# Kernel tuning notes

Hardware: AMD Instinct MI355X
Metric: run time of the kernel (lower is better)

## Reference

```python
import jax, jax.numpy as jnp
import numpy as np

B, T, D_IN, P, Q, D_OUT = 128, 1024, 64, 128, 2, 64


def _lstm_layer(x, w_ih, w_hh, b):
    """One LSTM layer, batch_first. x: [B,T,Din], w_ih: [4P,Din], w_hh: [4P,P], b: [4P].
    PyTorch gate order: i, f, g, o."""
    # Precompute input contribution for all timesteps (the big, parallel GEMM).
    gx = jnp.einsum('btd,gd->btg', x, w_ih) + b          # [B,T,4P]
    gx_t = jnp.swapaxes(gx, 0, 1)                        # [T,B,4P] for scan
    p = w_hh.shape[1]
    h0 = jnp.zeros((x.shape[0], p), dtype=x.dtype)
    c0 = jnp.zeros((x.shape[0], p), dtype=x.dtype)

    def step(carry, g_in):
        h, c = carry
        g = g_in + h @ w_hh.T                            # [B,4P]
        i, f, gg, o = jnp.split(g, 4, axis=-1)
        i = jax.nn.sigmoid(i)
        f = jax.nn.sigmoid(f)
        gg = jnp.tanh(gg)
        o = jax.nn.sigmoid(o)
        c = f * c + i * gg
        h = o * jnp.tanh(c)
        return (h, c), h

    _, hs = jax.lax.scan(step, (h0, c0), gx_t)           # hs: [T,B,P]
    return jnp.swapaxes(hs, 0, 1)                        # [B,T,P]


def setup_inputs() -> dict:
    key = jax.random.key(0)
    ks = jax.random.split(key, 8)
    x = jax.random.normal(ks[0], (B, T, D_IN), dtype=jnp.float32)
    # weight_ih: kaiming-normal-ish; weight_hh: orthogonal-ish (random normal is a fine stand-in
    # numerically; init distribution doesn't change the math being tested).
    w_ih0 = jax.random.normal(ks[1], (4 * P, D_IN), dtype=jnp.float32) * (1.0 / np.sqrt(D_IN))
    w_hh0 = jax.random.normal(ks[2], (4 * P, P), dtype=jnp.float32) * (1.0 / np.sqrt(P))
    w_ih1 = jax.random.normal(ks[3], (4 * P, P), dtype=jnp.float32) * (1.0 / np.sqrt(P))
    w_hh1 = jax.random.normal(ks[4], (4 * P, P), dtype=jnp.float32) * (1.0 / np.sqrt(P))
    # biases initialized to zero in the original (bias_ih + bias_hh folded into one per layer
    # would be equivalent math; keep both for faithfulness)
    b_ih = jnp.zeros((Q, 4 * P), dtype=jnp.float32)
    b_hh = jnp.zeros((Q, 4 * P), dtype=jnp.float32)
    fc_w = jax.random.normal(ks[5], (D_OUT, P), dtype=jnp.float32) * np.sqrt(2.0 / P)
    fc_b = jnp.zeros((D_OUT,), dtype=jnp.float32)
    return {"x": x, "w_ih0": w_ih0, "w_hh0": w_hh0, "w_ih1": w_ih1, "w_hh1": w_hh1,
            "b_ih": b_ih, "b_hh": b_hh, "fc_w": fc_w, "fc_b": fc_b}


def reference(x, w_ih0, w_hh0, w_ih1, w_hh1, b_ih, b_hh, fc_w, fc_b):
    h = _lstm_layer(x, w_ih0, w_hh0, b_ih[0] + b_hh[0])   # layer 0: [B,T,P]
    h = _lstm_layer(h, w_ih1, w_hh1, b_ih[1] + b_hh[1])   # layer 1: [B,T,P]
    return jnp.einsum('btp,op->bto', h, fc_w) + fc_b      # [B,T,D_OUT]
```

## Files before the change

### kernel.cpp

```cpp
#include <hip/hip_runtime.h>

#define NT 1024
#define RING 256
#define RMAR 24

typedef _Float16 half8 __attribute__((ext_vector_type(8)));
typedef _Float16 half4 __attribute__((ext_vector_type(4)));
typedef float f32x4 __attribute__((ext_vector_type(4)));

__device__ __forceinline__ f32x4 MFMA(half8 a, half8 b, f32x4 c) {
  return __builtin_amdgcn_mfma_f32_16x16x32_f16(a, b, c, 0, 0, 0);
}
__device__ __forceinline__ float sigf(float x) {
  return __builtin_amdgcn_rcpf(1.0f + __expf(-x));
}
__device__ __forceinline__ float tanhf2(float x) {
  float ax = fabsf(x);
  float e = __expf(-2.0f * ax);
  float t = (1.0f - e) * __builtin_amdgcn_rcpf(1.0f + e);
  return copysignf(t, x);
}
__device__ __forceinline__ half8 cvt8(float4 c0, float4 c1) {
  half8 hv;
  hv[0] = (_Float16)c0.x; hv[1] = (_Float16)c0.y;
  hv[2] = (_Float16)c0.z; hv[3] = (_Float16)c0.w;
  hv[4] = (_Float16)c1.x; hv[5] = (_Float16)c1.y;
  hv[6] = (_Float16)c1.z; hv[7] = (_Float16)c1.w;
  return hv;
}
struct U2 { unsigned long long a, b; };

__global__ __launch_bounds__(256) void prep_x(const float* __restrict__ x,
                                              _Float16* __restrict__ Xf) {
  int t0 = blockIdx.x * 256 + threadIdx.x;
  int l = t0 & 63;
  int fid = t0 >> 6;
  int kt = fid & 1;
  int t = (fid >> 1) & (NT - 1);
  int g = fid >> 11;
  int bt = g * 16 + (l & 15);
  int kb = kt * 32 + (l >> 4) * 4;
  const float* src = x + ((size_t)bt * NT + (size_t)t) * 64 + kb;
  float4 v0 = *(const float4*)src;
  float4 v1 = *(const float4*)(src + 16);
  *(half8*)(Xf + (size_t)fid * 512 + l * 8) = cvt8(v0, v1);
}

__global__ __launch_bounds__(512, 2) void lstm_main(
    const float* __restrict__ wih0, const float* __restrict__ whh0,
    const float* __restrict__ wih1, const float* __restrict__ whh1,
    const float* __restrict__ bih, const float* __restrict__ bhh,
    const float* __restrict__ fcw, const float* __restrict__ fcb,
    const _Float16* __restrict__ Xf, _Float16* __restrict__ ring,
    unsigned* __restrict__ prog, unsigned* __restrict__ consread,
    float* __restrict__ out) {
  const int tid = threadIdx.x;
  const int w = tid >> 6, l = tid & 63;
  const int n = l & 15, lg = l >> 4;
  const bool producer = blockIdx.x < 8;
  const int g = blockIdx.x & 7;

  __shared__ _Float16 hfrag[2][4][64][8];

  if (tid < 256) {
    half8 z = {0, 0, 0, 0, 0, 0, 0, 0};
    ((half8*)&hfrag[1][0][0][0])[tid] = z;
  }

  if (producer) {
    half8 A[4][6];
    f32x4 bias[4];
#pragma unroll
    for (int q = 0; q < 4; ++q) {
      int row = (w + 8 * q) * 16 + n;
#pragma unroll
      for (int kt = 0; kt < 6; ++kt) {
        int kb = kt * 32 + lg * 4;
        const float* wp = (kt < 2) ? (wih0 + (size_t)row * 64 + kb)
                                   : (whh0 + (size_t)row * 128 + (kb - 64));
        A[q][kt] = cvt8(*(const float4*)wp, *(const float4*)(wp + 16));
      }
      int rb = (w + 8 * q) * 16 + lg * 4;
      f32x4 bv;
#pragma unroll
      for (int r = 0; r < 4; ++r) bv[r] = bih[rb + r] + bhh[rb + r];
      bias[q] = bv;
    }
    const _Float16* XfG = Xf + (size_t)g * NT * 1024;
    _Float16* ringG = ring + (size_t)g * RING * 2048;
    half8 x0 = *(const half8*)(XfG + l * 8);
    half8 x1 = *(const half8*)(XfG + 512 + l * 8);
    f32x4 cst = {0.f, 0.f, 0.f, 0.f};
    unsigned Cc = 0;
    __syncthreads();
    for (int s = 0; s < NT; ++s) {
      half8 xn0, xn1;
      if (s + 1 < NT) {
        const _Float16* p = XfG + (size_t)(s + 1) * 1024 + l * 8;
        xn0 = *(const half8*)p;
        xn1 = *(const half8*)(p + 512);
      }
      if ((s & 7) == 0 && s >= RING - RMAR) {
        while (Cc + (RING - RMAR) <= (unsigned)s) {
          unsigned pv = 0;
          if (l == 0)
            pv = __hip_atomic_load(&consread[g], __ATOMIC_RELAXED,
                                   __HIP_MEMORY_SCOPE_AGENT);
          Cc = (unsigned)__builtin_amdgcn_readfirstlane((int)pv);
          if (Cc + (RING - RMAR) <= (unsigned)s) __builtin_amdgcn_s_sleep(8);
        }
      }
      f32x4 acc[4];
#pragma unroll
      for (int q = 0; q < 4; ++q) acc[q] = bias[q];
#pragma unroll
      for (int q = 0; q < 4; ++q) acc[q] = MFMA(A[q][0], x0, acc[q]);
#pragma unroll
      for (int q = 0; q < 4; ++q) acc[q] = MFMA(A[q][1], x1, acc[q]);
      const int rd = (s & 1) ^ 1;
#pragma unroll
      for (int kt = 0; kt < 4; ++kt) {
        half8 b = *(const half8*)&hfrag[rd][kt][l][0];
#pragma unroll
        for (int q = 0; q < 4; ++q) acc[q] = MFMA(A[q][2 + kt], b, acc[q]);
      }
      half4 hh;
#pragma unroll
      for (int r = 0; r < 4; ++r) {
        float iv = sigf(acc[0][r]), fv = sigf(acc[1][r]);
        float gv = tanhf2(acc[2][r]), ov = sigf(acc[3][r]);
        cst[r] = fv * cst[r] + iv * gv;
        hh[r] = (_Float16)(ov * tanhf2(cst[r]));
      }
      *(half4*)&hfrag[s & 1][w >> 1][l][(w & 1) * 4] = hh;
      unsigned long long uh = __builtin_bit_cast(unsigned long long, hh);
      unsigned long long* rp =
          (unsigned long long*)(ringG + (size_t)(s & (RING - 1)) * 2048 +
                                (w >> 1) * 512 + l * 8 + (w & 1) * 4);
      __hip_atomic_store(rp, uh, __ATOMIC_RELAXED, __HIP_MEMORY_SCOPE_AGENT);
      __syncthreads();
      if (tid == 0)
        __hip_atomic_store(&prog[g], (unsigned)(s + 1), __ATOMIC_RELEASE,
                           __HIP_MEMORY_SCOPE_AGENT);
      x0 = xn0;
      x1 = xn1;
    }
  } else {
    half8 A[4][8], FCA[4];
    f32x4 bias[4], fcbv = {0.f, 0.f, 0.f, 0.f};
    const bool W4 = (w < 4);
#pragma unroll
    for (int q = 0; q < 4; ++q) {
      int row = (w + 8 * q) * 16 + n;
#pragma unroll
      for (int kt = 0; kt < 8; ++kt) {
        int kb = kt * 32 + lg * 4;
        const float* wp = (kt < 4) ? (wih1 + (size_t)row * 128 + kb)
                                   : (whh1 + (size_t)row * 128 + (kb - 128));
        A[q][kt] = cvt8(*(const float4*)wp, *(const float4*)(wp + 16));
      }
      int rb = (w + 8 * q) * 16 + lg * 4;
      f32x4 bv;
#pragma unroll
      for (int r = 0; r < 4; ++r) bv[r] = bih[512 + rb + r] + bhh[512 + rb + r];
      bias[q] = bv;
    }
    if (W4) {
      int row = w * 16 + n;
#pragma unroll
      for (int kt = 0; kt < 4; ++kt) {
        int kb = kt * 32 + lg * 4;
        const float* wp = fcw + (size_t)row * 128 + kb;
        FCA[kt] = cvt8(*(const float4*)wp, *(const float4*)(wp + 16));
      }
      fcbv = *(const f32x4*)(fcb + w * 16 + lg * 4);
    }
    const _Float16* ringG = ring + (size_t)g * RING * 2048;
    unsigned Pc = 0;
    while (Pc < 1) {
      unsigned pv = 0;
      if (l == 0)
        pv = __hip_atomic_load(&prog[g], __ATOMIC_ACQUIRE,
                               __HIP_MEMORY_SCOPE_AGENT);
      Pc = (unsigned)__builtin_amdgcn_readfirstlane((int)pv);
      if (Pc < 1) __builtin_amdgcn_s_sleep(8);
    }
    half8 h0c[4];
#pragma unroll
    for (int kt = 0; kt < 4; ++kt) {
      const unsigned long long* rp =
          (const unsigned long long*)(ringG + kt * 512 + l * 8);
      U2 uu;
      uu.a = __hip_atomic_load(rp, __ATOMIC_RELAXED, __HIP_MEMORY_SCOPE_AGENT);
      uu.b = __hip_atomic_load(rp + 1, __ATOMIC_RELAXED, __HIP_MEMORY_SCOPE_AGENT);
      h0c[kt] = __builtin_bit_cast(half8, uu);
    }
    f32x4 cst = {0.f, 0.f, 0.f, 0.f};
    float* outG = out + ((size_t)(g * 16 + n) * NT) * 64 + w * 16 + lg * 4;
    __syncthreads();
    for (int s = 0; s <= NT; ++s) {
      f32x4 acc[4], afc = fcbv;
      if (s < NT) {
#pragma unroll
        for (int q = 0; q < 4; ++q) acc[q] = bias[q];
#pragma unroll
        for (int kt = 0; kt < 4; ++kt)
#pragma unroll
          for (int q = 0; q < 4; ++q) acc[q] = MFMA(A[q][kt], h0c[kt], acc[q]);
      }
      const int rd = (s & 1) ^ 1;
#pragma unroll
      for (int kt = 0; kt < 4; ++kt) {
        half8 b = *(const half8*)&hfrag[rd][kt][l][0];
        if (s < NT) {
#pragma unroll
          for (int q = 0; q < 4; ++q) acc[q] = MFMA(A[q][4 + kt], b, acc[q]);
        }
        if (W4) afc = MFMA(FCA[kt], b, afc);
      }
      if (W4 && s >= 1) *(f32x4*)(outG + (size_t)(s - 1) * 64) = afc;
      half8 h0n[4];
      if (s + 1 < NT) {
        while (Pc < (unsigned)(s + 2)) {
          unsigned pv = 0;
          if (l == 0)
            pv = __hip_atomic_load(&prog[g], __ATOMIC_ACQUIRE,
                                   __HIP_MEMORY_SCOPE_AGENT);
          Pc = (unsigned)__builtin_amdgcn_readfirstlane((int)pv);
          if (Pc < (unsigned)(s + 2)) __builtin_amdgcn_s_sleep(8);
        }
        const _Float16* rbase =
            ringG + (size_t)((s + 1) & (RING - 1)) * 2048 + l * 8;
#pragma unroll
        for (int kt = 0; kt < 4; ++kt) {
          const unsigned long long* rp =
              (const unsigned long long*)(rbase + kt * 512);
          U2 uu;
          uu.a = __hip_atomic_load(rp, __ATOMIC_RELAXED, __HIP_MEMORY_SCOPE_AGENT);
          uu.b = __hip_atomic_load(rp + 1, __ATOMIC_RELAXED, __HIP_MEMORY_SCOPE_AGENT);
          h0n[kt] = __builtin_bit_cast(half8, uu);
        }
      }
      if (s < NT) {
        half4 hh;
#pragma unroll
        for (int r = 0; r < 4; ++r) {
          float iv = sigf(acc[0][r]), fv = sigf(acc[1][r]);
          float gv = tanhf2(acc[2][r]), ov = sigf(acc[3][r]);
          cst[r] = fv * cst[r] + iv * gv;
          hh[r] = (_Float16)(ov * tanhf2(cst[r]));
        }
        *(half4*)&hfrag[s & 1][w >> 1][l][(w & 1) * 4] = hh;
      }
      if (tid == 0)
        __hip_atomic_store(&consread[g], (unsigned)(s + 1), __ATOMIC_RELAXED,
                           __HIP_MEMORY_SCOPE_AGENT);
      __syncthreads();
      if (s + 1 < NT) {
#pragma unroll
        for (int kt = 0; kt < 4; ++kt) h0c[kt] = h0n[kt];
      }
    }
  }
}

extern "C" void kernel_launch(void* const* d_in, const int* in_sizes, int n_in,
                              void* d_out, int out_size, void* d_ws, size_t ws_size,
                              hipStream_t stream) {
  const float* x     = (const float*)d_in[0];
  const float* w_ih0 = (const float*)d_in[1];
  const float* w_hh0 = (const float*)d_in[2];
  const float* w_ih1 = (const float*)d_in[3];
  const float* w_hh1 = (const float*)d_in[4];
  const float* b_ih  = (const float*)d_in[5];
  const float* b_hh  = (const float*)d_in[6];
  const float* fc_w  = (const float*)d_in[7];
  const float* fc_b  = (const float*)d_in[8];

  _Float16* Xf   = (_Float16*)d_ws;
  _Float16* ring = (_Float16*)((char*)d_ws + (16u << 20));
  unsigned* flags = (unsigned*)((char*)d_ws + (24u << 20));

  hipMemsetAsync(flags, 0, 64, stream);
  prep_x<<<4096, 256, 0, stream>>>(x, Xf);
  lstm_main<<<16, 512, 0, stream>>>(w_ih0, w_hh0, w_ih1, w_hh1, b_ih, b_hh,
                                    fc_w, fc_b, Xf, ring, flags, flags + 8,
                                    (float*)d_out);
}
```

Before: 1.474 ms.

## Split each LSTM layer's gate rows across two sibling workgroups

Each layer's recurrent step is now split across two 256-thread workgroups, each computing half of the hidden units (32 blocks instead of 16). Every step, the siblings exchange their half of h through global memory with per-step progress flags. This halves the per-workgroup MFMA and activation work on the serial critical path. In exchange it adds a cross-CU global round-trip and flag poll on every timestep, with shorter sleeps in polling. Ring backpressure checks are also relaxed to every 32 steps with a larger margin.

```diff
diff --git a/kernel.cpp b/kernel.cpp
--- a/kernel.cpp
+++ b/kernel.cpp
@@ -1,12 +1,14 @@
 #include <hip/hip_runtime.h>
 
 #define NT 1024
-#define RING 256
-#define RMAR 24
+#define RINGS 256
 
 typedef _Float16 half8 __attribute__((ext_vector_type(8)));
 typedef _Float16 half4 __attribute__((ext_vector_type(4)));
 typedef float f32x4 __attribute__((ext_vector_type(4)));
+typedef unsigned long long u64;
+
+struct U2 { u64 a, b; };
 
 __device__ __forceinline__ f32x4 MFMA(half8 a, half8 b, f32x4 c) {
   return __builtin_amdgcn_mfma_f32_16x16x32_f16(a, b, c, 0, 0, 0);
@@ -28,7 +30,25 @@
   hv[6] = (_Float16)c1.z; hv[7] = (_Float16)c1.w;
   return hv;
 }
-struct U2 { unsigned long long a, b; };
+__device__ __forceinline__ half8 ldring(const _Float16* p) {
+  const u64* q = (const u64*)p;
+  U2 uu;
+  uu.a = __hip_atomic_load(q, __ATOMIC_RELAXED, __HIP_MEMORY_SCOPE_AGENT);
+  uu.b = __hip_atomic_load(q + 1, __ATOMIC_RELAXED, __HIP_MEMORY_SCOPE_AGENT);
+  return __builtin_bit_cast(half8, uu);
+}
+__device__ __forceinline__ unsigned wpoll(unsigned* p, unsigned tgt,
+                                          unsigned cached, int l) {
+  unsigned c = cached;
+  while (c < tgt) {
+    unsigned pv = 0;
+    if (l == 0)
+      pv = __hip_atomic_load(p, __ATOMIC_ACQUIRE, __HIP_MEMORY_SCOPE_AGENT);
+    c = (unsigned)__builtin_amdgcn_readfirstlane((int)pv);
+    if (c < tgt) __builtin_amdgcn_s_sleep(2);
+  }
+  return c;
+}
 
 __global__ __launch_bounds__(256) void prep_x(const float* __restrict__ x,
                                               _Float16* __restrict__ Xf) {
@@ -46,52 +66,66 @@
   *(half8*)(Xf + (size_t)fid * 512 + l * 8) = cvt8(v0, v1);
 }
 
-__global__ __launch_bounds__(512, 2) void lstm_main(
+__global__ __launch_bounds__(256, 1) void lstm_main(
     const float* __restrict__ wih0, const float* __restrict__ whh0,
     const float* __restrict__ wih1, const float* __restrict__ whh1,
     const float* __restrict__ bih, const float* __restrict__ bhh,
     const float* __restrict__ fcw, const float* __restrict__ fcb,
-    const _Float16* __restrict__ Xf, _Float16* __restrict__ ring,
-    unsigned* __restrict__ prog, unsigned* __restrict__ consread,
+    const _Float16* __restrict__ Xf, _Float16* __restrict__ ringH0,
+    _Float16* __restrict__ h1x, unsigned* __restrict__ flags,
     float* __restrict__ out) {
   const int tid = threadIdx.x;
   const int w = tid >> 6, l = tid & 63;
   const int n = l & 15, lg = l >> 4;
-  const bool producer = blockIdx.x < 8;
+  const int role = blockIdx.x >> 3;
   const int g = blockIdx.x & 7;
-
-  __shared__ _Float16 hfrag[2][4][64][8];
-
-  if (tid < 256) {
+  const int half = role & 1;
+
+  __shared__ _Float16 hfr[2][2][64][8];
+  if (tid < 128) {
     half8 z = {0, 0, 0, 0, 0, 0, 0, 0};
-    ((half8*)&hfrag[1][0][0][0])[tid] = z;
+    ((half8*)&hfr[1][0][0][0])[tid] = z;
   }
-
-  if (producer) {
+  _Float16* ringG = ringH0 + (size_t)g * RINGS * 2048;
+  unsigned* fl = flags;
+#define FLAGP(st) (fl + ((st) * 8 + g) * 16)
+
+  const half8 hz = {0, 0, 0, 0, 0, 0, 0, 0};
+
+  if (role < 2) {
     half8 A[4][6];
     f32x4 bias[4];
 #pragma unroll
     for (int q = 0; q < 4; ++q) {
-      int row = (w + 8 * q) * 16 + n;
-#pragma unroll
-      for (int kt = 0; kt < 6; ++kt) {
-        int kb = kt * 32 + lg * 4;
-        const float* wp = (kt < 2) ? (wih0 + (size_t)row * 64 + kb)
-                                   : (whh0 + (size_t)row * 128 + (kb - 64));
+      int row = ((q << 3) + (half << 2) + w) * 16 + n;
+#pragma unroll
+      for (int kt = 0; kt < 2; ++kt) {
+        const float* wp = wih0 + (size_t)row * 64 + kt * 32 + lg * 4;
         A[q][kt] = cvt8(*(const float4*)wp, *(const float4*)(wp + 16));
       }
-      int rb = (w + 8 * q) * 16 + lg * 4;
+#pragma unroll
+      for (int kt = 0; kt < 4; ++kt) {
+        const float* wp = whh0 + (size_t)row * 128 + kt * 32 + lg * 4;
+        A[q][2 + kt] = cvt8(*(const float4*)wp, *(const float4*)(wp + 16));
+      }
+      int rb = ((q << 3) + (half << 2) + w) * 16 + lg * 4;
       f32x4 bv;
 #pragma unroll
       for (int r = 0; r < 4; ++r) bv[r] = bih[rb + r] + bhh[rb + r];
       bias[q] = bv;
     }
+    unsigned* progSelf = FLAGP(half);
+    unsigned* progSib = FLAGP(half ^ 1);
+    unsigned* consA = FLAGP(2);
+    unsigned* consB = FLAGP(3);
+    const int ownK = half << 1;
+    const int remK = (half ^ 1) << 1;
     const _Float16* XfG = Xf + (size_t)g * NT * 1024;
-    _Float16* ringG = ring + (size_t)g * RING * 2048;
     half8 x0 = *(const half8*)(XfG + l * 8);
     half8 x1 = *(const half8*)(XfG + 512 + l * 8);
+    half8 h0r0 = hz, h0r1 = hz;
     f32x4 cst = {0.f, 0.f, 0.f, 0.f};
-    unsigned Cc = 0;
+    unsigned PcS = 0, PcA = 0, PcB = 0;
     __syncthreads();
     for (int s = 0; s < NT; ++s) {
       half8 xn0, xn1;
@@ -100,29 +134,28 @@
         xn0 = *(const half8*)p;
         xn1 = *(const half8*)(p + 512);
       }
-      if ((s & 7) == 0 && s >= RING - RMAR) {
-        while (Cc + (RING - RMAR) <= (unsigned)s) {
-          unsigned pv = 0;
-          if (l == 0)
-            pv = __hip_atomic_load(&consread[g], __ATOMIC_RELAXED,
-                                   __HIP_MEMORY_SCOPE_AGENT);
-          Cc = (unsigned)__builtin_amdgcn_readfirstlane((int)pv);
-          if (Cc + (RING - RMAR) <= (unsigned)s) __builtin_amdgcn_s_sleep(8);
-        }
-      }
+      if ((s & 31) == 0 && s >= RINGS - 64) {
+        unsigned tgt = (unsigned)(s - (RINGS - 64)) + 1;
+        PcA = wpoll(consA, tgt, PcA, l);
+        PcB = wpoll(consB, tgt, PcB, l);
+      }
+      half8 bo0 = *(const half8*)&hfr[(s + 1) & 1][0][l][0];
+      half8 bo1 = *(const half8*)&hfr[(s + 1) & 1][1][l][0];
+      half8 b2 = (half == 0) ? bo0 : h0r0;
+      half8 b3 = (half == 0) ? bo1 : h0r1;
+      half8 b4 = (half == 0) ? h0r0 : bo0;
+      half8 b5 = (half == 0) ? h0r1 : bo1;
       f32x4 acc[4];
 #pragma unroll
-      for (int q = 0; q < 4; ++q) acc[q] = bias[q];
-#pragma unroll
-      for (int q = 0; q < 4; ++q) acc[q] = MFMA(A[q][0], x0, acc[q]);
-#pragma unroll
-      for (int q = 0; q < 4; ++q) acc[q] = MFMA(A[q][1], x1, acc[q]);
-      const int rd = (s & 1) ^ 1;
-#pragma unroll
-      for (int kt = 0; kt < 4; ++kt) {
-        half8 b = *(const half8*)&hfrag[rd][kt][l][0];
-#pragma unroll
-        for (int q = 0; q < 4; ++q) acc[q] = MFMA(A[q][2 + kt], b, acc[q]);
+      for (int q = 0; q < 4; ++q) {
+        f32x4 a = bias[q];
+        a = MFMA(A[q][0], x0, a);
+        a = MFMA(A[q][1], x1, a);
+        a = MFMA(A[q][2], b2, a);
+        a = MFMA(A[q][3], b3, a);
+        a = MFMA(A[q][4], b4, a);
+        a = MFMA(A[q][5], b5, a);
+        acc[q] = a;
       }
       half4 hh;
 #pragma unroll
@@ -132,116 +165,118 @@
         cst[r] = fv * cst[r] + iv * gv;
         hh[r] = (_Float16)(ov * tanhf2(cst[r]));
       }
-      *(half4*)&hfrag[s & 1][w >> 1][l][(w & 1) * 4] = hh;
-      unsigned long long uh = __builtin_bit_cast(unsigned long long, hh);
-      unsigned long long* rp =
-          (unsigned long long*)(ringG + (size_t)(s & (RING - 1)) * 2048 +
-                                (w >> 1) * 512 + l * 8 + (w & 1) * 4);
-      __hip_atomic_store(rp, uh, __ATOMIC_RELAXED, __HIP_MEMORY_SCOPE_AGENT);
+      *(half4*)&hfr[s & 1][w >> 1][l][(w & 1) << 2] = hh;
+      u64 uh = __builtin_bit_cast(u64, hh);
+      __hip_atomic_store(
+          (u64*)(ringG + (size_t)(s & (RINGS - 1)) * 2048 +
+                 (ownK + (w >> 1)) * 512 + l * 8 + (w & 1) * 4),
+          uh, __ATOMIC_RELAXED, __HIP_MEMORY_SCOPE_AGENT);
       __syncthreads();
       if (tid == 0)
-        __hip_atomic_store(&prog[g], (unsigned)(s + 1), __ATOMIC_RELEASE,
+        __hip_atomic_store(progSelf, (unsigned)(s + 1), __ATOMIC_RELEASE,
                            __HIP_MEMORY_SCOPE_AGENT);
-      x0 = xn0;
-      x1 = xn1;
+      if (s + 1 < NT) {
+        PcS = wpoll(progSib, (unsigned)(s + 1), PcS, l);
+        const _Float16* rb2 =
+            ringG + (size_t)(s & (RINGS - 1)) * 2048 + remK * 512 + l * 8;
+        h0r0 = ldring(rb2);
+        h0r1 = ldring(rb2 + 512);
+        x0 = xn0;
+        x1 = xn1;
+      }
     }
   } else {
     half8 A[4][8], FCA[4];
     f32x4 bias[4], fcbv = {0.f, 0.f, 0.f, 0.f};
-    const bool W4 = (w < 4);
 #pragma unroll
     for (int q = 0; q < 4; ++q) {
-      int row = (w + 8 * q) * 16 + n;
-#pragma unroll
-      for (int kt = 0; kt < 8; ++kt) {
-        int kb = kt * 32 + lg * 4;
-        const float* wp = (kt < 4) ? (wih1 + (size_t)row * 128 + kb)
-                                   : (whh1 + (size_t)row * 128 + (kb - 128));
+      int row = ((q << 3) + (half << 2) + w) * 16 + n;
+#pragma unroll
+      for (int kt = 0; kt < 4; ++kt) {
+        const float* wp = wih1 + (size_t)row * 128 + kt * 32 + lg * 4;
         A[q][kt] = cvt8(*(const float4*)wp, *(const float4*)(wp + 16));
       }
-      int rb = (w + 8 * q) * 16 + lg * 4;
+#pragma unroll
+      for (int kt = 0; kt < 4; ++kt) {
+        const float* wp = whh1 + (size_t)row * 128 + kt * 32 + lg * 4;
+        A[q][4 + kt] = cvt8(*(const float4*)wp, *(const float4*)(wp + 16));
+      }
+      int rb = ((q << 3) + (half << 2) + w) * 16 + lg * 4;
       f32x4 bv;
 #pragma unroll
-      for (int r = 0; r < 4; ++r) bv[r] = bih[512 + rb + r] + bhh[512 + rb + r];
+      for (int r = 0; r < 4; ++r)
+        bv[r] = bih[512 + rb + r] + bhh[512 + rb + r];
       bias[q] = bv;
     }
-    if (W4) {
-      int row = w * 16 + n;
+    if (half == 1) {
+      int frow = (w << 4) + n;
 #pragma unroll
       for (int kt = 0; kt < 4; ++kt) {
-        int kb = kt * 32 + lg * 4;
-        const float* wp = fcw + (size_t)row * 128 + kb;
+        const float* wp = fcw + (size_t)frow * 128 + kt * 32 + lg * 4;
         FCA[kt] = cvt8(*(const float4*)wp, *(const float4*)(wp + 16));
       }
-      fcbv = *(const f32x4*)(fcb + w * 16 + lg * 4);
-    }
-    const _Float16* ringG = ring + (size_t)g * RING * 2048;
-    unsigned Pc = 0;
-    while (Pc < 1) {
-      unsigned pv = 0;
-      if (l == 0)
-        pv = __hip_atomic_load(&prog[g], __ATOMIC_ACQUIRE,
-                               __HIP_MEMORY_SCOPE_AGENT);
-      Pc = (unsigned)__builtin_amdgcn_readfirstlane((int)pv);
-      if (Pc < 1) __builtin_amdgcn_s_sleep(8);
-    }
-    half8 h0c[4];
-#pragma unroll
-    for (int kt = 0; kt < 4; ++kt) {
-      const unsigned long long* rp =
-          (const unsigned long long*)(ringG + kt * 512 + l * 8);
-      U2 uu;
-      uu.a = __hip_atomic_load(rp, __ATOMIC_RELAXED, __HIP_MEMORY_SCOPE_AGENT);
-      uu.b = __hip_atomic_load(rp + 1, __ATOMIC_RELAXED, __HIP_MEMORY_SCOPE_AGENT);
-      h0c[kt] = __builtin_bit_cast(half8, uu);
-    }
+      fcbv = *(const f32x4*)(fcb + (w << 4) + lg * 4);
+    }
+    unsigned* progSelf = FLAGP(2 + half);
+    unsigned* progSib = FLAGP(2 + (half ^ 1));
+    unsigned* pL0a = FLAGP(0);
+    unsigned* pL0b = FLAGP(1);
+    _Float16* sx = h1x + (size_t)((half << 3) + g) * 4096;
+    _Float16* rx = h1x + (size_t)(((half ^ 1) << 3) + g) * 4096;
+    unsigned PcS = 0, PcA = 0, PcB = 0;
+    PcA = wpoll(pL0a, 1, 0, l);
+    PcB = wpoll(pL0b, 1, 0, l);
+    half8 h0c0 = ldring(ringG + l * 8);
+    half8 h0c1 = ldring(ringG + 512 + l * 8);
+    half8 h0c2 = ldring(ringG + 1024 + l * 8);
+    half8 h0c3 = ldring(ringG + 1536 + l * 8);
+    half8 h1r0 = hz, h1r1 = hz;
     f32x4 cst = {0.f, 0.f, 0.f, 0.f};
-    float* outG = out + ((size_t)(g * 16 + n) * NT) * 64 + w * 16 + lg * 4;
+    float* outG = out + (size_t)((g << 4) + n) * NT * 64 + (w << 4) + lg * 4;
     __syncthreads();
-    for (int s = 0; s <= NT; ++s) {
-      f32x4 acc[4], afc = fcbv;
-      if (s < NT) {
-#pragma unroll
-        for (int q = 0; q < 4; ++q) acc[q] = bias[q];
-#pragma unroll
-        for (int kt = 0; kt < 4; ++kt)
-#pragma unroll
-          for (int q = 0; q < 4; ++q) acc[q] = MFMA(A[q][kt], h0c[kt], acc[q]);
-      }
-      const int rd = (s & 1) ^ 1;
-#pragma unroll
-      for (int kt = 0; kt < 4; ++kt) {
-        half8 b = *(const half8*)&hfrag[rd][kt][l][0];
-        if (s < NT) {
-#pragma unroll
-          for (int q = 0; q < 4; ++q) acc[q] = MFMA(A[q][4 + kt], b, acc[q]);
+    for (int t = 0; t <= NT; ++t) {
+      half8 bo0 = *(const half8*)&hfr[(t + 1) & 1][0][l][0];
+      half8 bo1 = *(const half8*)&hfr[(t + 1) & 1][1][l][0];
+      f32x4 acc[4];
+      if (t < NT) {
+        half8 b4 = (half == 0) ? bo0 : h1r0;
+        half8 b5 = (half == 0) ? bo1 : h1r1;
+        half8 b6 = (half == 0) ? h1r0 : bo0;
+        half8 b7 = (half == 0) ? h1r1 : bo1;
+#pragma unroll
+        for (int q = 0; q < 4; ++q) {
+          f32x4 a = bias[q];
+          a = MFMA(A[q][0], h0c0, a);
+          a = MFMA(A[q][1], h0c1, a);
+          a = MFMA(A[q][2], h0c2, a);
+          a = MFMA(A[q][3], h0c3, a);
+          a = MFMA(A[q][4], b4, a);
+          a = MFMA(A[q][5], b5, a);
+          a = MFMA(A[q][6], b6, a);
+          a = MFMA(A[q][7], b7, a);
+          acc[q] = a;
         }
-        if (W4) afc = MFMA(FCA[kt], b, afc);
-      }
-      if (W4 && s >= 1) *(f32x4*)(outG + (size_t)(s - 1) * 64) = afc;
-      half8 h0n[4];
-      if (s + 1 < NT) {
-        while (Pc < (unsigned)(s + 2)) {
-          unsigned pv = 0;
-          if (l == 0)
-            pv = __hip_atomic_load(&prog[g], __ATOMIC_ACQUIRE,
-                                   __HIP_MEMORY_SCOPE_AGENT);
-          Pc = (unsigned)__builtin_amdgcn_readfirstlane((int)pv);
-          if (Pc < (unsigned)(s + 2)) __builtin_amdgcn_s_sleep(8);
-        }
-        const _Float16* rbase =
-            ringG + (size_t)((s + 1) & (RING - 1)) * 2048 + l * 8;
-#pragma unroll
-        for (int kt = 0; kt < 4; ++kt) {
-          const unsigned long long* rp =
-              (const unsigned long long*)(rbase + kt * 512);
-          U2 uu;
-          uu.a = __hip_atomic_load(rp, __ATOMIC_RELAXED, __HIP_MEMORY_SCOPE_AGENT);
-          uu.b = __hip_atomic_load(rp + 1, __ATOMIC_RELAXED, __HIP_MEMORY_SCOPE_AGENT);
-          h0n[kt] = __builtin_bit_cast(half8, uu);
-        }
-      }
-      if (s < NT) {
+      }
+      if (half == 1 && t >= 1) {
+        f32x4 afc = fcbv;
+        afc = MFMA(FCA[0], h1r0, afc);
+        afc = MFMA(FCA[1], h1r1, afc);
+        afc = MFMA(FCA[2], bo0, afc);
+        afc = MFMA(FCA[3], bo1, afc);
+        *(f32x4*)(outG + (size_t)(t - 1) * 64) = afc;
+      }
+      half8 h0n0, h0n1, h0n2, h0n3;
+      if (t + 1 < NT) {
+        if (PcA < (unsigned)(t + 2)) PcA = wpoll(pL0a, t + 2, PcA, l);
+        if (PcB < (unsigned)(t + 2)) PcB = wpoll(pL0b, t + 2, PcB, l);
+        const _Float16* rb2 =
+            ringG + (size_t)((t + 1) & (RINGS - 1)) * 2048 + l * 8;
+        h0n0 = ldring(rb2);
+        h0n1 = ldring(rb2 + 512);
+        h0n2 = ldring(rb2 + 1024);
+        h0n3 = ldring(rb2 + 1536);
+      }
+      if (t < NT) {
         half4 hh;
 #pragma unroll
         for (int r = 0; r < 4; ++r) {
@@ -250,18 +285,28 @@
           cst[r] = fv * cst[r] + iv * gv;
           hh[r] = (_Float16)(ov * tanhf2(cst[r]));
         }
-        *(half4*)&hfrag[s & 1][w >> 1][l][(w & 1) * 4] = hh;
-      }
+        *(half4*)&hfr[t & 1][w >> 1][l][(w & 1) << 2] = hh;
+        u64 uh = __builtin_bit_cast(u64, hh);
+        __hip_atomic_store((u64*)(sx + (size_t)(t & 3) * 1024 +
+                                  (w >> 1) * 512 + l * 8 + (w & 1) * 4),
+                           uh, __ATOMIC_RELAXED, __HIP_MEMORY_SCOPE_AGENT);
+      }
+      __syncthreads();
       if (tid == 0)
-        __hip_atomic_store(&consread[g], (unsigned)(s + 1), __ATOMIC_RELAXED,
+        __hip_atomic_store(progSelf, (unsigned)(t + 1), __ATOMIC_RELEASE,
                            __HIP_MEMORY_SCOPE_AGENT);
-      __syncthreads();
-      if (s + 1 < NT) {
-#pragma unroll
-        for (int kt = 0; kt < 4; ++kt) h0c[kt] = h0n[kt];
+      if (t < NT) {
+        PcS = wpoll(progSib, (unsigned)(t + 1), PcS, l);
+        const _Float16* xb = rx + (size_t)(t & 3) * 1024 + l * 8;
+        h1r0 = ldring(xb);
+        h1r1 = ldring(xb + 512);
+      }
+      if (t + 1 < NT) {
+        h0c0 = h0n0; h0c1 = h0n1; h0c2 = h0n2; h0c3 = h0n3;
       }
     }
   }
+#undef FLAGP
 }
 
 extern "C" void kernel_launch(void* const* d_in, const int* in_sizes, int n_in,
@@ -279,11 +324,12 @@
 
   _Float16* Xf   = (_Float16*)d_ws;
   _Float16* ring = (_Float16*)((char*)d_ws + (16u << 20));
-  unsigned* flags = (unsigned*)((char*)d_ws + (24u << 20));
-
-  hipMemsetAsync(flags, 0, 64, stream);
+  _Float16* h1x  = (_Float16*)((char*)d_ws + (24u << 20));
+  unsigned* flags = (unsigned*)((char*)d_ws + (24u << 20) + (256u << 10));
+
+  hipMemsetAsync(flags, 0, 4096, stream);
   prep_x<<<4096, 256, 0, stream>>>(x, Xf);
-  lstm_main<<<16, 512, 0, stream>>>(w_ih0, w_hh0, w_ih1, w_hh1, b_ih, b_hh,
-                                    fc_w, fc_b, Xf, ring, flags, flags + 8,
+  lstm_main<<<32, 256, 0, stream>>>(w_ih0, w_hh0, w_ih1, w_hh1, b_ih, b_hh,
+                                    fc_w, fc_b, Xf, ring, h1x, flags,
                                     (float*)d_out);
 }
```

Result: slower. 3.063 ms (+107.9%).
